# Performance work log

Measured on AMD Instinct MI355X. Metric: run time of the kernel, lower is better.

Reference implementation:

```python
import jax, jax.numpy as jnp
import numpy as np

THRESH = 0.5
MARGIN = 0.1
SCALE_POS = 2.0
SCALE_NEG = 40.0
EPSILON = 1e-5


def setup_inputs() -> dict:
    key = jax.random.key(0)
    kx, kl = jax.random.split(key)
    B, D, N_CLASSES = 4096, 1024, 256
    x = jax.random.normal(kx, (B, D), dtype=jnp.float32)
    # L2-normalize embeddings (standard for multi-similarity loss; keeps sim in [-1, 1])
    x = x / jnp.linalg.norm(x, axis=1, keepdims=True)
    labels = jax.random.randint(kl, (B,), 0, N_CLASSES, dtype=jnp.int64)
    return {"x": x, "labels": labels}


def reference(x, labels):
    B = x.shape[0]
    sim = jnp.matmul(x, x.T)  # [B, B]

    eye = jnp.eye(B, dtype=bool)
    same = labels[:, None] == labels[None, :]
    pos_mask = same & ~eye                      # positives excl. self
    neg_mask = ~same                            # negatives
    pos_valid = pos_mask & (sim < 1.0 - EPSILON)  # pos_pair_ after < 1-eps filter

    # per-row hardest stats (inf/-inf where empty)
    min_pos = jnp.min(jnp.where(pos_valid, sim, jnp.inf), axis=1)   # min over pos_pair_
    max_neg = jnp.max(jnp.where(neg_mask, sim, -jnp.inf), axis=1)   # max over neg_pair_

    # mined pairs
    neg_keep = neg_mask & (sim + MARGIN > min_pos[:, None])
    pos_keep = pos_valid & (sim - MARGIN < max_neg[:, None])

    has_row = (pos_valid.any(axis=1) & neg_mask.any(axis=1)
               & pos_keep.any(axis=1) & neg_keep.any(axis=1))

    pos_sum = jnp.sum(jnp.where(pos_keep, jnp.exp(-SCALE_POS * (sim - THRESH)), 0.0), axis=1)
    neg_sum = jnp.sum(jnp.where(neg_keep, jnp.exp(SCALE_NEG * (sim - THRESH)), 0.0), axis=1)

    pos_loss = jnp.log1p(pos_sum) / SCALE_POS
    neg_loss = jnp.log1p(neg_sum) / SCALE_NEG

    row_loss = jnp.where(has_row, pos_loss + neg_loss, 0.0)
    return jnp.sum(row_loss) / B
```

## Files before the change

kernel.cpp:

```cpp
#include <hip/hip_runtime.h>
#include <hip/hip_bf16.h>
#include <math.h>
#include <stdint.h>


#define THRESH    0.5f
#define MARGIN    0.1f
#define SCALE_POS 2.0f
#define SCALE_NEG 40.0f
#define POS_CAP   (1.0f - 1e-5f)

typedef __bf16 bf16x8 __attribute__((ext_vector_type(8)));
typedef float  f32x4  __attribute__((ext_vector_type(4)));

__device__ __forceinline__ uint16_t f2bf(float f) {
  union { float f; uint32_t u; } v; v.f = f;
  uint32_t u = v.u;
  u += 0x7FFFu + ((u >> 16) & 1u);
  return (uint16_t)(u >> 16);
}

__device__ __forceinline__ uint32_t fenc(float f) {
  union { float f; uint32_t u; } v; v.f = f;
  return (v.u & 0x80000000u) ? ~v.u : (v.u ^ 0x80000000u);
}
__device__ __forceinline__ float fdec(uint32_t k) {
  union { float f; uint32_t u; } v;
  v.u = (k & 0x80000000u) ? (k ^ 0x80000000u) : ~k;
  return v.f;
}

__global__ __launch_bounds__(256) void cvt_bf16_kernel(
    const float* __restrict__ x, uint16_t* __restrict__ y, int n) {
  int i = (blockIdx.x * 256 + threadIdx.x) * 4;
  if (i + 3 < n) {
    float4 v = *(const float4*)(x + i);
    ushort4 o;
    o.x = f2bf(v.x); o.y = f2bf(v.y); o.z = f2bf(v.z); o.w = f2bf(v.w);
    *(ushort4*)(y + i) = o;
  }
}

#if defined(__has_builtin)
#if __has_builtin(__builtin_amdgcn_global_load_lds)
#define HAVE_GLL 1
#endif
#endif

__device__ __forceinline__ void stage16(const uint16_t* g, uint16_t* lds_wave_base, int lane) {
#ifdef HAVE_GLL
  __builtin_amdgcn_global_load_lds(
      (const __attribute__((address_space(1))) void*)g,
      (__attribute__((address_space(3))) void*)lds_wave_base, 16, 0, 0);
#else
  *(uint4*)(lds_wave_base + lane * 8) = *(const uint4*)g;
#endif
}

__global__ __launch_bounds__(256) void simgemm_kernel(
    const uint16_t* __restrict__ X, const int* __restrict__ labels,
    float* __restrict__ C, uint32_t* __restrict__ gmin, uint32_t* __restrict__ gmax,
    int B, int D) {
  __shared__ __align__(16) uint16_t sT[2][2][128 * 64];
  __shared__ int slabR[128];
  __shared__ int slabC[128];

  const int nblk = B >> 7;
  const int nb   = nblk * (nblk + 1) / 2;

  int t = blockIdx.x;
  if ((nb & 7) == 0) {
    const int cpx = nb >> 3;
    t = (t % 8) * cpx + t / 8;
  }
  int bi = 0;
  while (t >= nblk - bi) { t -= nblk - bi; ++bi; }
  const int bj = bi + t;
  const int bm = bi * 128;
  const int bn = bj * 128;

  const int tid  = threadIdx.x;
  const int wave = tid >> 6;
  const int lane = tid & 63;
  const int waveM = wave >> 1, waveN = wave & 1;

  if (tid < 128) slabR[tid] = labels[bm + tid];
  else           slabC[tid - 128] = labels[bn + tid - 128];

  const uint16_t* gA = X + (size_t)bm * D;
  const uint16_t* gB = X + (size_t)bn * D;

  int srcOff[4];
#pragma unroll
  for (int s = 0; s < 4; ++s) {
    const int idx = s * 256 + tid;
    const int row = idx >> 3;
    const int cb  = ((idx & 7) << 4) ^ ((row & 7) << 4);
    srcOff[s] = row * D + (cb >> 1);
  }

  const int fr = lane & 15;
  const int fq = lane >> 4;
  const int sw = (fr & 7) << 4;

  f32x4 acc[4][4] = {};

  const int NT = D >> 6;

#pragma unroll
  for (int s = 0; s < 4; ++s) {
    uint16_t* dA = &sT[0][0][0] + (s * 256 + wave * 64) * 8;
    uint16_t* dB = &sT[0][1][0] + (s * 256 + wave * 64) * 8;
    stage16(gA + srcOff[s], dA, lane);
    stage16(gB + srcOff[s], dB, lane);
  }
  __syncthreads();

  int cur = 0;
  for (int kt = 0; kt < NT; ++kt) {
    if (kt + 1 < NT) {
      const int k0 = (kt + 1) << 6;
#pragma unroll
      for (int s = 0; s < 4; ++s) {
        uint16_t* dA = &sT[cur ^ 1][0][0] + (s * 256 + wave * 64) * 8;
        uint16_t* dB = &sT[cur ^ 1][1][0] + (s * 256 + wave * 64) * 8;
        stage16(gA + srcOff[s] + k0, dA, lane);
        stage16(gB + srcOff[s] + k0, dB, lane);
      }
    }

    const char* tA = (const char*)&sT[cur][0][0];
    const char* tB = (const char*)&sT[cur][1][0];
#pragma unroll
    for (int kk = 0; kk < 2; ++kk) {
      const int cbyte = (kk * 64 + fq * 16) ^ sw;
      bf16x8 af[4], bfv[4];
#pragma unroll
      for (int mt = 0; mt < 4; ++mt) {
        const int rowa = waveM * 64 + mt * 16 + fr;
        af[mt] = *(const bf16x8*)(tA + rowa * 128 + cbyte);
      }
#pragma unroll
      for (int nt = 0; nt < 4; ++nt) {
        const int rowb = waveN * 64 + nt * 16 + fr;
        bfv[nt] = *(const bf16x8*)(tB + rowb * 128 + cbyte);
      }
#pragma unroll
      for (int mt = 0; mt < 4; ++mt)
#pragma unroll
        for (int nt = 0; nt < 4; ++nt)
          acc[mt][nt] = __builtin_amdgcn_mfma_f32_16x16x32_bf16(
              af[mt], bfv[nt], acc[mt][nt], 0, 0, 0);
    }

    __syncthreads();
    cur ^= 1;
  }

#pragma unroll
  for (int mt = 0; mt < 4; ++mt) {
#pragma unroll
    for (int nt = 0; nt < 4; ++nt) {
      const int col = bn + waveN * 64 + nt * 16 + fr;
#pragma unroll
      for (int r = 0; r < 4; ++r) {
        const int row = bm + waveM * 64 + mt * 16 + fq * 4 + r;
        C[(size_t)row * B + col] = acc[mt][nt][r];
      }
    }
  }

  if (bi != bj) {
#pragma unroll
    for (int mt = 0; mt < 4; ++mt) {
#pragma unroll
      for (int nt = 0; nt < 4; ++nt) {
        const int col  = bn + waveN * 64 + nt * 16 + fr;
        const int rowb = bm + waveM * 64 + mt * 16 + fq * 4;
        *(f32x4*)(C + (size_t)col * B + rowb) = acc[mt][nt];
      }
    }
  }

  const float INF = __builtin_inff();

  int lr[4][4];
#pragma unroll
  for (int mt = 0; mt < 4; ++mt)
#pragma unroll
    for (int r = 0; r < 4; ++r)
      lr[mt][r] = slabR[waveM * 64 + mt * 16 + fq * 4 + r];
  int lc[4];
#pragma unroll
  for (int nt = 0; nt < 4; ++nt) lc[nt] = slabC[waveN * 64 + nt * 16 + fr];

  {
    float rmin[4][4], rmax[4][4];
#pragma unroll
    for (int mt = 0; mt < 4; ++mt)
#pragma unroll
      for (int r = 0; r < 4; ++r) { rmin[mt][r] = INF; rmax[mt][r] = -INF; }

#pragma unroll
    for (int mt = 0; mt < 4; ++mt) {
#pragma unroll
      for (int nt = 0; nt < 4; ++nt) {
        const int gcol = bn + waveN * 64 + nt * 16 + fr;
#pragma unroll
        for (int r = 0; r < 4; ++r) {
          const int grow = bm + waveM * 64 + mt * 16 + fq * 4 + r;
          const float s = acc[mt][nt][r];
          if (lr[mt][r] == lc[nt]) {
            if (grow != gcol && s < POS_CAP) rmin[mt][r] = fminf(rmin[mt][r], s);
          } else {
            rmax[mt][r] = fmaxf(rmax[mt][r], s);
          }
        }
      }
    }
#pragma unroll
    for (int mt = 0; mt < 4; ++mt)
#pragma unroll
      for (int r = 0; r < 4; ++r) {
#pragma unroll
        for (int m = 1; m < 16; m <<= 1) {
          rmin[mt][r] = fminf(rmin[mt][r], __shfl_xor(rmin[mt][r], m, 64));
          rmax[mt][r] = fmaxf(rmax[mt][r], __shfl_xor(rmax[mt][r], m, 64));
        }
      }
    if (fr == 0) {
#pragma unroll
      for (int mt = 0; mt < 4; ++mt)
#pragma unroll
        for (int r = 0; r < 4; ++r) {
          const int grow = bm + waveM * 64 + mt * 16 + fq * 4 + r;
          if (rmin[mt][r] < INF)  atomicMin(&gmin[grow], fenc(rmin[mt][r]));
          if (rmax[mt][r] > -INF) atomicMax(&gmax[grow], fenc(rmax[mt][r]));
        }
    }
  }

  if (bi != bj) {
    float cmin[4], cmax[4];
#pragma unroll
    for (int nt = 0; nt < 4; ++nt) { cmin[nt] = INF; cmax[nt] = -INF; }

#pragma unroll
    for (int nt = 0; nt < 4; ++nt) {
      const int gcol = bn + waveN * 64 + nt * 16 + fr;
#pragma unroll
      for (int mt = 0; mt < 4; ++mt) {
#pragma unroll
        for (int r = 0; r < 4; ++r) {
          const int grow = bm + waveM * 64 + mt * 16 + fq * 4 + r;
          const float s = acc[mt][nt][r];
          if (lc[nt] == lr[mt][r]) {
            if (grow != gcol && s < POS_CAP) cmin[nt] = fminf(cmin[nt], s);
          } else {
            cmax[nt] = fmaxf(cmax[nt], s);
          }
        }
      }
    }
#pragma unroll
    for (int nt = 0; nt < 4; ++nt) {
#pragma unroll
      for (int m = 16; m < 64; m <<= 1) {
        cmin[nt] = fminf(cmin[nt], __shfl_xor(cmin[nt], m, 64));
        cmax[nt] = fmaxf(cmax[nt], __shfl_xor(cmax[nt], m, 64));
      }
    }
    if (fq == 0) {
#pragma unroll
      for (int nt = 0; nt < 4; ++nt) {
        const int gcol = bn + waveN * 64 + nt * 16 + fr;
        if (cmin[nt] < INF)  atomicMin(&gmin[gcol], fenc(cmin[nt]));
        if (cmax[nt] > -INF) atomicMax(&gmax[gcol], fenc(cmax[nt]));
      }
    }
  }
}

__global__ __launch_bounds__(256) void rowloss_kernel(
    const float* __restrict__ sim, const int* __restrict__ labels,
    const uint32_t* __restrict__ gmin, const uint32_t* __restrict__ gmax,
    float* __restrict__ rowbuf, int B) {
  __shared__ int   slab[4096];
  __shared__ float red[8];

  const int tid  = threadIdx.x;
  const int wave = tid >> 6;
  const int lane = tid & 63;
  const float INF = __builtin_inff();

  for (int tq = tid; tq < (B >> 2); tq += 256)
    ((int4*)slab)[tq] = ((const int4*)labels)[tq];
  __syncthreads();

  const int iters = B >> 10;
  for (int rr = 0; rr < 4; ++rr) {
    const int i = blockIdx.x * 4 + rr;
    const float* row = sim + (size_t)i * B;
    const int li = slab[i];

    const uint32_t kmin = gmin[i], kmax = gmax[i];
    const bool haspos = (kmin != 0xFFFFFFFFu);
    const bool hasneg = (kmax != 0u);
    const float minpos = haspos ? fdec(kmin) : INF;
    const float maxneg = hasneg ? fdec(kmax) : -INF;

    float psum = 0.f, nsum = 0.f;
    for (int it = 0; it < iters; ++it) {
      const int j = it * 1024 + tid * 4;
      float4 v = *(const float4*)(row + j);
      float s4[4] = {v.x, v.y, v.z, v.w};
#pragma unroll
      for (int q = 0; q < 4; ++q) {
        const int jj = j + q;
        const float s = s4[q];
        if (slab[jj] == li) {
          if (jj != i && s < POS_CAP && (s - MARGIN < maxneg))
            psum += __expf(-SCALE_POS * (s - THRESH));
        } else {
          if (s + MARGIN > minpos)
            nsum += __expf(SCALE_NEG * (s - THRESH));
        }
      }
    }

#pragma unroll
    for (int m = 32; m > 0; m >>= 1) {
      psum += __shfl_xor(psum, m, 64);
      nsum += __shfl_xor(nsum, m, 64);
    }
    if (lane == 0) { red[wave] = psum; red[4 + wave] = nsum; }
    __syncthreads();

    if (tid == 0) {
      psum = red[0] + red[1] + red[2] + red[3];
      nsum = red[4] + red[5] + red[6] + red[7];
      const bool has_row = haspos && hasneg && (psum > 0.f) && (nsum > 0.f);
      rowbuf[i] = has_row
          ? (log1pf(psum) * (1.0f / SCALE_POS) + log1pf(nsum) * (1.0f / SCALE_NEG))
          : 0.f;
    }
    __syncthreads();
  }
}

__global__ __launch_bounds__(256) void finalreduce_kernel(
    const float* __restrict__ rowbuf, float* __restrict__ out, int B) {
  __shared__ float red[4];
  const int tid  = threadIdx.x;
  const int wave = tid >> 6;
  const int lane = tid & 63;

  float s = 0.f;
  for (int j = tid * 4; j < B; j += 1024) {
    float4 v = *(const float4*)(rowbuf + j);
    s += v.x + v.y + v.z + v.w;
  }
#pragma unroll
  for (int m = 32; m > 0; m >>= 1) s += __shfl_xor(s, m, 64);
  if (lane == 0) red[wave] = s;
  __syncthreads();
  if (tid == 0)
    out[0] = (red[0] + red[1] + red[2] + red[3]) * (1.0f / (float)B);
}

extern "C" void kernel_launch(void* const* d_in, const int* in_sizes, int n_in,
                              void* d_out, int out_size, void* d_ws, size_t ws_size,
                              hipStream_t stream) {
  const float* x      = (const float*)d_in[0];
  const int*   labels = (const int*)d_in[1];
  float*       out    = (float*)d_out;

  const int B = in_sizes[1];
  const int D = in_sizes[0] / B;

  uint16_t* xbf = (uint16_t*)d_ws;
  size_t xbytes = (((size_t)B * D * 2) + 255) & ~(size_t)255;
  float* sim = (float*)((char*)d_ws + xbytes);
  size_t simbytes = (size_t)B * B * 4;
  float* rowbuf = (float*)((char*)d_ws + xbytes + simbytes);
  uint32_t* gmin = (uint32_t*)((char*)d_ws + xbytes + simbytes + (size_t)B * 4);
  uint32_t* gmax = (uint32_t*)((char*)d_ws + xbytes + simbytes + (size_t)B * 8);

  hipMemsetAsync(gmin, 0xFF, (size_t)B * 4, stream);
  hipMemsetAsync(gmax, 0x00, (size_t)B * 4, stream);

  const int n = B * D;
  cvt_bf16_kernel<<<n / 1024, 256, 0, stream>>>(x, xbf, n);

  const int nblk = B / 128;
  const int nb   = nblk * (nblk + 1) / 2;
  simgemm_kernel<<<nb, 256, 0, stream>>>(xbf, labels, sim, gmin, gmax, B, D);

  rowloss_kernel<<<B / 4, 256, 0, stream>>>(sim, labels, gmin, gmax, rowbuf, B);
  finalreduce_kernel<<<1, 256, 0, stream>>>(rowbuf, out, B);
}
```

Baseline: 148.1 us.

## Recompute similarity GEMM in second pass instead of materializing BxB matrix

The full 4096x4096 fp32 similarity matrix is no longer written and re-read. The symmetric bf16 GEMM now runs twice. The first pass computes per-row hardest positive and negative stats with atomics. The second pass recomputes the tile and accumulates the mined exp sums for both rows and columns into per-block partial buffers, which a small kernel then reduces per row. This trades roughly 128 MB of global memory traffic for a second GEMM's compute.

After: 209.5 us. 41.5% more time.

```diff
diff --git a/kernel.cpp b/kernel.cpp
--- a/kernel.cpp
+++ b/kernel.cpp
@@ -57,13 +57,18 @@
 #endif
 }
 
-__global__ __launch_bounds__(256) void simgemm_kernel(
+template <int PASS>
+__global__ __launch_bounds__(256) void simgemm_fused(
     const uint16_t* __restrict__ X, const int* __restrict__ labels,
-    float* __restrict__ C, uint32_t* __restrict__ gmin, uint32_t* __restrict__ gmax,
+    uint32_t* __restrict__ gmin, uint32_t* __restrict__ gmax,
+    float* __restrict__ psum_part, float* __restrict__ nsum_part,
     int B, int D) {
   __shared__ __align__(16) uint16_t sT[2][2][128 * 64];
   __shared__ int slabR[128];
   __shared__ int slabC[128];
+  __shared__ float sMinR[128], sMaxR[128], sMinC[128], sMaxC[128];
+  __shared__ float psumR[2][128], nsumR[2][128];
+  __shared__ float psumC[2][128], nsumC[2][128];
 
   const int nblk = B >> 7;
   const int nb   = nblk * (nblk + 1) / 2;
@@ -157,31 +162,6 @@
     cur ^= 1;
   }
 
-#pragma unroll
-  for (int mt = 0; mt < 4; ++mt) {
-#pragma unroll
-    for (int nt = 0; nt < 4; ++nt) {
-      const int col = bn + waveN * 64 + nt * 16 + fr;
-#pragma unroll
-      for (int r = 0; r < 4; ++r) {
-        const int row = bm + waveM * 64 + mt * 16 + fq * 4 + r;
-        C[(size_t)row * B + col] = acc[mt][nt][r];
-      }
-    }
-  }
-
-  if (bi != bj) {
-#pragma unroll
-    for (int mt = 0; mt < 4; ++mt) {
-#pragma unroll
-      for (int nt = 0; nt < 4; ++nt) {
-        const int col  = bn + waveN * 64 + nt * 16 + fr;
-        const int rowb = bm + waveM * 64 + mt * 16 + fq * 4;
-        *(f32x4*)(C + (size_t)col * B + rowb) = acc[mt][nt];
-      }
-    }
-  }
-
   const float INF = __builtin_inff();
 
   int lr[4][4];
@@ -194,7 +174,7 @@
 #pragma unroll
   for (int nt = 0; nt < 4; ++nt) lc[nt] = slabC[waveN * 64 + nt * 16 + fr];
 
-  {
+  if constexpr (PASS == 1) {
     float rmin[4][4], rmax[4][4];
 #pragma unroll
     for (int mt = 0; mt < 4; ++mt)
@@ -238,114 +218,172 @@
           if (rmax[mt][r] > -INF) atomicMax(&gmax[grow], fenc(rmax[mt][r]));
         }
     }
-  }
-
-  if (bi != bj) {
-    float cmin[4], cmax[4];
-#pragma unroll
-    for (int nt = 0; nt < 4; ++nt) { cmin[nt] = INF; cmax[nt] = -INF; }
-
-#pragma unroll
-    for (int nt = 0; nt < 4; ++nt) {
-      const int gcol = bn + waveN * 64 + nt * 16 + fr;
-#pragma unroll
-      for (int mt = 0; mt < 4; ++mt) {
-#pragma unroll
-        for (int r = 0; r < 4; ++r) {
-          const int grow = bm + waveM * 64 + mt * 16 + fq * 4 + r;
-          const float s = acc[mt][nt][r];
-          if (lc[nt] == lr[mt][r]) {
-            if (grow != gcol && s < POS_CAP) cmin[nt] = fminf(cmin[nt], s);
-          } else {
-            cmax[nt] = fmaxf(cmax[nt], s);
-          }
-        }
-      }
-    }
-#pragma unroll
-    for (int nt = 0; nt < 4; ++nt) {
-#pragma unroll
-      for (int m = 16; m < 64; m <<= 1) {
-        cmin[nt] = fminf(cmin[nt], __shfl_xor(cmin[nt], m, 64));
-        cmax[nt] = fmaxf(cmax[nt], __shfl_xor(cmax[nt], m, 64));
-      }
-    }
-    if (fq == 0) {
+
+    if (bi != bj) {
+      float cmin[4], cmax[4];
+#pragma unroll
+      for (int nt = 0; nt < 4; ++nt) { cmin[nt] = INF; cmax[nt] = -INF; }
 #pragma unroll
       for (int nt = 0; nt < 4; ++nt) {
         const int gcol = bn + waveN * 64 + nt * 16 + fr;
-        if (cmin[nt] < INF)  atomicMin(&gmin[gcol], fenc(cmin[nt]));
-        if (cmax[nt] > -INF) atomicMax(&gmax[gcol], fenc(cmax[nt]));
-      }
-    }
-  }
-}
-
-__global__ __launch_bounds__(256) void rowloss_kernel(
-    const float* __restrict__ sim, const int* __restrict__ labels,
+#pragma unroll
+        for (int mt = 0; mt < 4; ++mt) {
+#pragma unroll
+          for (int r = 0; r < 4; ++r) {
+            const int grow = bm + waveM * 64 + mt * 16 + fq * 4 + r;
+            const float s = acc[mt][nt][r];
+            if (lc[nt] == lr[mt][r]) {
+              if (grow != gcol && s < POS_CAP) cmin[nt] = fminf(cmin[nt], s);
+            } else {
+              cmax[nt] = fmaxf(cmax[nt], s);
+            }
+          }
+        }
+      }
+#pragma unroll
+      for (int nt = 0; nt < 4; ++nt) {
+#pragma unroll
+        for (int m = 16; m < 64; m <<= 1) {
+          cmin[nt] = fminf(cmin[nt], __shfl_xor(cmin[nt], m, 64));
+          cmax[nt] = fmaxf(cmax[nt], __shfl_xor(cmax[nt], m, 64));
+        }
+      }
+      if (fq == 0) {
+#pragma unroll
+        for (int nt = 0; nt < 4; ++nt) {
+          const int gcol = bn + waveN * 64 + nt * 16 + fr;
+          if (cmin[nt] < INF)  atomicMin(&gmin[gcol], fenc(cmin[nt]));
+          if (cmax[nt] > -INF) atomicMax(&gmax[gcol], fenc(cmax[nt]));
+        }
+      }
+    }
+  } else {
+    if (tid < 128) {
+      const uint32_t km = gmin[bm + tid], kx = gmax[bm + tid];
+      sMinR[tid] = (km == 0xFFFFFFFFu) ? INF : fdec(km);
+      sMaxR[tid] = (kx == 0u) ? -INF : fdec(kx);
+    } else {
+      const int rr = tid - 128;
+      const uint32_t km = gmin[bn + rr], kx = gmax[bn + rr];
+      sMinC[rr] = (km == 0xFFFFFFFFu) ? INF : fdec(km);
+      sMaxC[rr] = (kx == 0u) ? -INF : fdec(kx);
+    }
+    __syncthreads();
+
+    const bool offd = (bi != bj);
+
+    float minC[4], maxC[4];
+#pragma unroll
+    for (int nt = 0; nt < 4; ++nt) {
+      const int cloc = waveN * 64 + nt * 16 + fr;
+      minC[nt] = sMinC[cloc];
+      maxC[nt] = sMaxC[cloc];
+    }
+
+    float lp[4][4] = {}, ln_[4][4] = {};
+    float lpc[4] = {}, lnc[4] = {};
+
+#pragma unroll
+    for (int mt = 0; mt < 4; ++mt) {
+#pragma unroll
+      for (int r = 0; r < 4; ++r) {
+        const int rloc = waveM * 64 + mt * 16 + fq * 4 + r;
+        const int grow = bm + rloc;
+        const float mR = sMinR[rloc];
+        const float xR = sMaxR[rloc];
+        const int   la = lr[mt][r];
+#pragma unroll
+        for (int nt = 0; nt < 4; ++nt) {
+          const int gcol = bn + waveN * 64 + nt * 16 + fr;
+          const float s = acc[mt][nt][r];
+          const bool same = (la == lc[nt]);
+          const bool posv = same && (grow != gcol) && (s < POS_CAP);
+          const bool negv = !same;
+          const float ep = __expf(-SCALE_POS * (s - THRESH));
+          const float en = __expf( SCALE_NEG * (s - THRESH));
+          if (posv && (s - MARGIN < xR)) lp[mt][r]  += ep;
+          if (negv && (s + MARGIN > mR)) ln_[mt][r] += en;
+          if (offd) {
+            if (posv && (s - MARGIN < maxC[nt])) lpc[nt] += ep;
+            if (negv && (s + MARGIN > minC[nt])) lnc[nt] += en;
+          }
+        }
+      }
+    }
+
+#pragma unroll
+    for (int mt = 0; mt < 4; ++mt)
+#pragma unroll
+      for (int r = 0; r < 4; ++r) {
+#pragma unroll
+        for (int m = 1; m < 16; m <<= 1) {
+          lp[mt][r]  += __shfl_xor(lp[mt][r],  m, 64);
+          ln_[mt][r] += __shfl_xor(ln_[mt][r], m, 64);
+        }
+      }
+    if (fr == 0) {
+#pragma unroll
+      for (int mt = 0; mt < 4; ++mt)
+#pragma unroll
+        for (int r = 0; r < 4; ++r) {
+          const int rloc = waveM * 64 + mt * 16 + fq * 4 + r;
+          psumR[waveN][rloc] = lp[mt][r];
+          nsumR[waveN][rloc] = ln_[mt][r];
+        }
+    }
+
+    if (offd) {
+#pragma unroll
+      for (int nt = 0; nt < 4; ++nt) {
+#pragma unroll
+        for (int m = 16; m < 64; m <<= 1) {
+          lpc[nt] += __shfl_xor(lpc[nt], m, 64);
+          lnc[nt] += __shfl_xor(lnc[nt], m, 64);
+        }
+      }
+      if (fq == 0) {
+#pragma unroll
+        for (int nt = 0; nt < 4; ++nt) {
+          const int cloc = waveN * 64 + nt * 16 + fr;
+          psumC[waveM][cloc] = lpc[nt];
+          nsumC[waveM][cloc] = lnc[nt];
+        }
+      }
+    }
+    __syncthreads();
+
+    if (tid < 128) {
+      const float p = psumR[0][tid] + psumR[1][tid];
+      const float n = nsumR[0][tid] + nsumR[1][tid];
+      psum_part[(size_t)(bm + tid) * nblk + bj] = p;
+      nsum_part[(size_t)(bm + tid) * nblk + bj] = n;
+    } else if (offd) {
+      const int rr = tid - 128;
+      const float p = psumC[0][rr] + psumC[1][rr];
+      const float n = nsumC[0][rr] + nsumC[1][rr];
+      psum_part[(size_t)(bn + rr) * nblk + bi] = p;
+      nsum_part[(size_t)(bn + rr) * nblk + bi] = n;
+    }
+  }
+}
+
+__global__ __launch_bounds__(256) void rowfinal_kernel(
     const uint32_t* __restrict__ gmin, const uint32_t* __restrict__ gmax,
-    float* __restrict__ rowbuf, int B) {
-  __shared__ int   slab[4096];
-  __shared__ float red[8];
-
-  const int tid  = threadIdx.x;
-  const int wave = tid >> 6;
-  const int lane = tid & 63;
-  const float INF = __builtin_inff();
-
-  for (int tq = tid; tq < (B >> 2); tq += 256)
-    ((int4*)slab)[tq] = ((const int4*)labels)[tq];
-  __syncthreads();
-
-  const int iters = B >> 10;
-  for (int rr = 0; rr < 4; ++rr) {
-    const int i = blockIdx.x * 4 + rr;
-    const float* row = sim + (size_t)i * B;
-    const int li = slab[i];
-
-    const uint32_t kmin = gmin[i], kmax = gmax[i];
-    const bool haspos = (kmin != 0xFFFFFFFFu);
-    const bool hasneg = (kmax != 0u);
-    const float minpos = haspos ? fdec(kmin) : INF;
-    const float maxneg = hasneg ? fdec(kmax) : -INF;
-
-    float psum = 0.f, nsum = 0.f;
-    for (int it = 0; it < iters; ++it) {
-      const int j = it * 1024 + tid * 4;
-      float4 v = *(const float4*)(row + j);
-      float s4[4] = {v.x, v.y, v.z, v.w};
-#pragma unroll
-      for (int q = 0; q < 4; ++q) {
-        const int jj = j + q;
-        const float s = s4[q];
-        if (slab[jj] == li) {
-          if (jj != i && s < POS_CAP && (s - MARGIN < maxneg))
-            psum += __expf(-SCALE_POS * (s - THRESH));
-        } else {
-          if (s + MARGIN > minpos)
-            nsum += __expf(SCALE_NEG * (s - THRESH));
-        }
-      }
-    }
-
-#pragma unroll
-    for (int m = 32; m > 0; m >>= 1) {
-      psum += __shfl_xor(psum, m, 64);
-      nsum += __shfl_xor(nsum, m, 64);
-    }
-    if (lane == 0) { red[wave] = psum; red[4 + wave] = nsum; }
-    __syncthreads();
-
-    if (tid == 0) {
-      psum = red[0] + red[1] + red[2] + red[3];
-      nsum = red[4] + red[5] + red[6] + red[7];
-      const bool has_row = haspos && hasneg && (psum > 0.f) && (nsum > 0.f);
-      rowbuf[i] = has_row
-          ? (log1pf(psum) * (1.0f / SCALE_POS) + log1pf(nsum) * (1.0f / SCALE_NEG))
-          : 0.f;
-    }
-    __syncthreads();
-  }
+    const float* __restrict__ psum_part, const float* __restrict__ nsum_part,
+    float* __restrict__ rowbuf, int B, int nblk) {
+  const int i = blockIdx.x * 256 + threadIdx.x;
+  if (i >= B) return;
+  float ps = 0.f, ns = 0.f;
+  for (int q = 0; q < nblk; ++q) {
+    ps += psum_part[(size_t)i * nblk + q];
+    ns += nsum_part[(size_t)i * nblk + q];
+  }
+  const bool haspos = (gmin[i] != 0xFFFFFFFFu);
+  const bool hasneg = (gmax[i] != 0u);
+  const bool has_row = haspos && hasneg && (ps > 0.f) && (ns > 0.f);
+  rowbuf[i] = has_row
+      ? (log1pf(ps) * (1.0f / SCALE_POS) + log1pf(ns) * (1.0f / SCALE_NEG))
+      : 0.f;
 }
 
 __global__ __launch_bounds__(256) void finalreduce_kernel(
@@ -377,14 +415,15 @@
 
   const int B = in_sizes[1];
   const int D = in_sizes[0] / B;
-
-  uint16_t* xbf = (uint16_t*)d_ws;
-  size_t xbytes = (((size_t)B * D * 2) + 255) & ~(size_t)255;
-  float* sim = (float*)((char*)d_ws + xbytes);
-  size_t simbytes = (size_t)B * B * 4;
-  float* rowbuf = (float*)((char*)d_ws + xbytes + simbytes);
-  uint32_t* gmin = (uint32_t*)((char*)d_ws + xbytes + simbytes + (size_t)B * 4);
-  uint32_t* gmax = (uint32_t*)((char*)d_ws + xbytes + simbytes + (size_t)B * 8);
+  const int nblk = B / 128;
+
+  char* ws = (char*)d_ws;
+  uint16_t* xbf = (uint16_t*)ws;                 ws += (((size_t)B * D * 2) + 255) & ~(size_t)255;
+  uint32_t* gmin = (uint32_t*)ws;                ws += (size_t)B * 4;
+  uint32_t* gmax = (uint32_t*)ws;                ws += (size_t)B * 4;
+  float* psum_part = (float*)ws;                 ws += (size_t)B * nblk * 4;
+  float* nsum_part = (float*)ws;                 ws += (size_t)B * nblk * 4;
+  float* rowbuf = (float*)ws;                    ws += (size_t)B * 4;
 
   hipMemsetAsync(gmin, 0xFF, (size_t)B * 4, stream);
   hipMemsetAsync(gmax, 0x00, (size_t)B * 4, stream);
@@ -392,10 +431,13 @@
   const int n = B * D;
   cvt_bf16_kernel<<<n / 1024, 256, 0, stream>>>(x, xbf, n);
 
-  const int nblk = B / 128;
-  const int nb   = nblk * (nblk + 1) / 2;
-  simgemm_kernel<<<nb, 256, 0, stream>>>(xbf, labels, sim, gmin, gmax, B, D);
-
-  rowloss_kernel<<<B / 4, 256, 0, stream>>>(sim, labels, gmin, gmax, rowbuf, B);
+  const int nb = nblk * (nblk + 1) / 2;
+  simgemm_fused<1><<<nb, 256, 0, stream>>>(xbf, labels, gmin, gmax,
+                                           psum_part, nsum_part, B, D);
+  simgemm_fused<2><<<nb, 256, 0, stream>>>(xbf, labels, gmin, gmax,
+                                           psum_part, nsum_part, B, D);
+
+  rowfinal_kernel<<<(B + 255) / 256, 256, 0, stream>>>(gmin, gmax, psum_part,
+                                                       nsum_part, rowbuf, B, nblk);
   finalreduce_kernel<<<1, 256, 0, stream>>>(rowbuf, out, B);
 }
```
